# Performance work log

Measured on AMD Instinct MI355X. Metric: run time of the kernel, lower is better.

## Reference

```python
import jax, jax.numpy as jnp
import numpy as np

B, S, D = 2, 2048, 2048
H = 16
KV_RANK, Q_RANK = 512, 1536
NOPE, ROPE_D, VD = 128, 64, 128
QK_D = NOPE + ROPE_D  # 192


def _rope(t, positions):
    # t: (B, H, S, d) with d even; rotate-half RoPE, theta=10000
    d = t.shape[-1]
    inv_freq = 1.0 / (10000.0 ** (jnp.arange(0, d, 2, dtype=jnp.float32) / d))
    ang = positions.astype(jnp.float32)[:, None] * inv_freq  # (S, d//2)
    cos, sin = jnp.cos(ang), jnp.sin(ang)                    # (S, d//2)
    t1, t2 = t[..., : d // 2], t[..., d // 2 :]
    return jnp.concatenate([t1 * cos - t2 * sin, t2 * cos + t1 * sin], axis=-1)


def setup_inputs() -> dict:
    key = jax.random.key(0)
    ks = jax.random.split(key, 10)
    sc = 0.02
    return {
        "x": jax.random.normal(ks[0], (B, S, D), dtype=jnp.float32),
        "positions": jnp.arange(S, dtype=jnp.int32),
        # torch.nn.Linear weights are (out_features, in_features)
        "Wq_down": jax.random.normal(ks[1], (Q_RANK, D), dtype=jnp.float32) * sc,
        "Wq_up": jax.random.normal(ks[2], (H * NOPE, Q_RANK), dtype=jnp.float32) * sc,
        "Wq_rope": jax.random.normal(ks[3], (H * ROPE_D, Q_RANK), dtype=jnp.float32) * sc,
        "Wkv_down": jax.random.normal(ks[4], (KV_RANK, D), dtype=jnp.float32) * sc,
        "Wk_up": jax.random.normal(ks[5], (H * NOPE, KV_RANK), dtype=jnp.float32) * sc,
        "Wv_up": jax.random.normal(ks[6], (H * VD, KV_RANK), dtype=jnp.float32) * sc,
        "Wk_rope": jax.random.normal(ks[7], (ROPE_D, D), dtype=jnp.float32) * sc,
        "Wo": jax.random.normal(ks[8], (D, H * VD), dtype=jnp.float32) * sc,
    }


def reference(x, positions, Wq_down, Wq_up, Wq_rope, Wkv_down, Wk_up, Wv_up, Wk_rope, Wo):
    bsz, seq_len, _ = x.shape

    # Query path: low-rank down, then nope + rope up-projections
    c_q = x @ Wq_down.T                                             # (B, S, Q_RANK)
    q_c = (c_q @ Wq_up.T).reshape(bsz, seq_len, H, NOPE).transpose(0, 2, 1, 3)
    q_r = (c_q @ Wq_rope.T).reshape(bsz, seq_len, H, ROPE_D).transpose(0, 2, 1, 3)
    q_r = _rope(q_r, positions)
    q = jnp.concatenate([q_c, q_r], axis=-1)                        # (B, H, S, QK_D)

    # KV path: shared latent, single rope head broadcast to all heads
    c_kv = x @ Wkv_down.T                                           # (B, S, KV_RANK)
    k_c = (c_kv @ Wk_up.T).reshape(bsz, seq_len, H, NOPE).transpose(0, 2, 1, 3)
    v_c = (c_kv @ Wv_up.T).reshape(bsz, seq_len, H, VD).transpose(0, 2, 1, 3)
    k_r = (x @ Wk_rope.T).reshape(bsz, seq_len, 1, ROPE_D).transpose(0, 2, 1, 3)
    k_r = _rope(k_r, positions)
    k_r = jnp.broadcast_to(k_r, (bsz, H, seq_len, ROPE_D))
    k = jnp.concatenate([k_c, k_r], axis=-1)                        # (B, H, S, QK_D)

    # Causal SDPA, scale = 1/sqrt(total qk head dim)
    scale = 1.0 / math.sqrt(QK_D) if False else QK_D ** -0.5
    scores = jnp.einsum("bhqd,bhkd->bhqk", q, k) * scale
    causal = jnp.tril(jnp.ones((seq_len, seq_len), dtype=bool))
    scores = jnp.where(causal, scores, jnp.finfo(scores.dtype).min)
    attn = jax.nn.softmax(scores, axis=-1)
    out = jnp.einsum("bhqk,bhkd->bhqd", attn, v_c)                  # (B, H, S, VD)

    out = out.transpose(0, 2, 1, 3).reshape(bsz, seq_len, H * VD)
    return out @ Wo.T                                               # (B, S, D)
```

## Files before the change

kernel.cpp:

```cpp
#include <hip/hip_runtime.h>
#include <cmath>

#define SLEN 2048

typedef __bf16 bf16x8 __attribute__((ext_vector_type(8)));
typedef float  f32x4  __attribute__((ext_vector_type(4)));

__device__ inline void gld16(const void* g, void* l) {
    __builtin_amdgcn_global_load_lds(
        (const __attribute__((address_space(1))) void*)(uintptr_t)g,
        (__attribute__((address_space(3))) void*)(unsigned)(uintptr_t)l, 16, 0, 0);
}

struct CvArgs {
    const float* src[9];
    __bf16*      dst[9];
    long         cum[10];
};
__global__ __launch_bounds__(256)
void convert_all(CvArgs a) {
    long i8 = ((long)blockIdx.x * 256 + threadIdx.x) * 8;
    if (i8 >= a.cum[9]) return;
    int s = 0;
#pragma unroll
    for (int k = 1; k < 9; k++) if (i8 >= a.cum[k]) s = k;
    long loc = i8 - a.cum[s];
    const float* sp = a.src[s] + loc;
    float4 u0 = *(const float4*)(sp);
    float4 u1 = *(const float4*)(sp + 4);
    bf16x8 o;
    o[0] = (__bf16)u0.x; o[1] = (__bf16)u0.y; o[2] = (__bf16)u0.z; o[3] = (__bf16)u0.w;
    o[4] = (__bf16)u1.x; o[5] = (__bf16)u1.y; o[6] = (__bf16)u1.z; o[7] = (__bf16)u1.w;
    *(bf16x8*)(a.dst[s] + loc) = o;
}

struct Outs { __bf16* a; __bf16* b; __bf16* c; float* f; };

__global__ __launch_bounds__(256, 2)
void gemm_nt(const __bf16* __restrict__ A, const __bf16* __restrict__ B,
             Outs o, const int* __restrict__ positions,
             int M, int N, int K, int mode, float scale) {
    __shared__ __bf16 As[128 * 64];
    __shared__ __bf16 Bs[128 * 64];
    int tid = threadIdx.x;
    int wave = tid >> 6, lane = tid & 63;
    int lane15 = lane & 15, quad = lane >> 4;
    int ri = lane >> 3, ci = lane & 7;
    int cg = ci ^ ri;
    int m0 = blockIdx.x * 128, n0 = blockIdx.y * 128;
    int wm = (wave & 1) * 64, wn = (wave >> 1) * 64;
    f32x4 acc[4][4] = {};

    for (int k0 = 0; k0 < K; k0 += 64) {
#pragma unroll
        for (int t = 0; t < 4; t++) {
            int rr = wave * 32 + t * 8;
            int r = rr + ri;
            gld16(A + (size_t)(m0 + r) * K + k0 + cg * 8, As + rr * 64);
            int br = n0 + r; if (br > N - 1) br = N - 1;
            gld16(B + (size_t)br * K + k0 + cg * 8, Bs + rr * 64);
        }
        __syncthreads();
#pragma unroll
        for (int kk = 0; kk < 64; kk += 32) {
            int jb = kk >> 3;
            bf16x8 af[4], bfr[4];
#pragma unroll
            for (int mt = 0; mt < 4; mt++) {
                int rA = wm + mt * 16 + lane15;
                af[mt] = *(bf16x8*)(As + rA * 64 + (((jb + quad) ^ (rA & 7)) << 3));
            }
#pragma unroll
            for (int nt = 0; nt < 4; nt++) {
                int rB = wn + nt * 16 + lane15;
                bfr[nt] = *(bf16x8*)(Bs + rB * 64 + (((jb + quad) ^ (rB & 7)) << 3));
            }
#pragma unroll
            for (int mt = 0; mt < 4; mt++)
#pragma unroll
                for (int nt = 0; nt < 4; nt++)
                    acc[mt][nt] = __builtin_amdgcn_mfma_f32_16x16x32_bf16(
                        af[mt], bfr[nt], acc[mt][nt], 0, 0, 0);
        }
        __syncthreads();
    }

    const float KLOG = 13.287712379549449f / 32.0f;

    if (mode == 8 && n0 == 2048) {
        if (wn == 0) {
#pragma unroll
            for (int mt = 0; mt < 4; mt++) {
                int row = m0 + wm + mt * 16 + quad * 4;
#pragma unroll
                for (int nt = 0; nt < 2; nt++) {
                    int i = nt * 16 + lane15;
                    float inv = exp2f(-(float)i * KLOG);
#pragma unroll
                    for (int r = 0; r < 4; r++) {
                        int tok = row + r;
                        float p = (float)positions[tok & (SLEN - 1)];
                        float sn, cs; sincosf(p * inv, &sn, &cs);
                        float t1 = acc[mt][nt][r], t2 = acc[mt][nt + 2][r];
                        float rot1 = t1 * cs - t2 * sn;
                        float rot2 = t2 * cs + t1 * sn;
                        size_t ob = (size_t)tok * 3072 + 128;
#pragma unroll
                        for (int hh = 0; hh < 16; hh++) {
                            o.c[ob + hh * 192 + i]      = (__bf16)rot1;
                            o.c[ob + hh * 192 + 32 + i] = (__bf16)rot2;
                        }
                    }
                }
            }
        }
        return;
    }
    if (mode == 9 && n0 >= 2048) {
        int hh = (n0 + wn - 2048) >> 6;
#pragma unroll
        for (int mt = 0; mt < 4; mt++) {
            int row = m0 + wm + mt * 16 + quad * 4;
#pragma unroll
            for (int nt = 0; nt < 2; nt++) {
                int i = nt * 16 + lane15;
                float inv = exp2f(-(float)i * KLOG);
#pragma unroll
                for (int r = 0; r < 4; r++) {
                    int tok = row + r;
                    float p = (float)positions[tok & (SLEN - 1)];
                    float sn, cs; sincosf(p * inv, &sn, &cs);
                    float t1 = acc[mt][nt][r], t2 = acc[mt][nt + 2][r];
                    size_t ob = (size_t)tok * 3072 + hh * 192 + 128;
                    o.a[ob + i]      = (__bf16)((t1 * cs - t2 * sn) * scale);
                    o.a[ob + 32 + i] = (__bf16)((t2 * cs + t1 * sn) * scale);
                }
            }
        }
        return;
    }

#pragma unroll
    for (int mt = 0; mt < 4; mt++) {
        int row = m0 + wm + mt * 16 + quad * 4;
#pragma unroll
        for (int nt = 0; nt < 4; nt++) {
            int col = n0 + wn + nt * 16 + lane15;
            if (col < N) {
#pragma unroll
                for (int r = 0; r < 4; r++) {
                    float v = acc[mt][nt][r];
                    size_t rw = (size_t)(row + r);
                    if (mode == 2) {
                        o.f[rw * N + col] = v;
                    } else if (mode == 8) {
                        if (col < 1536) o.a[rw * 1536 + col] = (__bf16)v;
                        else            o.b[rw * 512 + col - 1536] = (__bf16)v;
                    } else if (mode == 9) {
                        o.a[rw * 3072 + (col >> 7) * 192 + (col & 127)] =
                            (__bf16)(v * scale);
                    } else {
                        if (col < 2048)
                            o.a[rw * 3072 + (col >> 7) * 192 + (col & 127)] = (__bf16)v;
                        else {
                            int d = col - 2048;
                            o.b[((size_t)d * 2 + (rw >> 11)) * 2048 + (rw & 2047)] = (__bf16)v;
                        }
                    }
                }
            }
        }
    }
}

__global__ __launch_bounds__(256, 2)
void mla_attn(const __bf16* __restrict__ Q, const __bf16* __restrict__ K,
              const __bf16* __restrict__ Vt, __bf16* __restrict__ O) {
    __shared__ __bf16 Ks[64 * 192];
    __shared__ __bf16 Vs[128 * 64];
    __shared__ __bf16 Ps[4][32][72];
    int tid = threadIdx.x, wave = tid >> 6, lane = tid & 63;
    int lane15 = lane & 15, quad = lane >> 4;
    int h = blockIdx.y, b = blockIdx.z;
    int x = blockIdx.x;
    int qt0 = (x & 1) ? (x >> 1) : (15 - (x >> 1));
    int qt = b ? (15 - qt0) : qt0;
    int q0 = qt * 128;
    const __bf16* Qb  = Q + (size_t)b * SLEN * 3072 + h * 192;
    const __bf16* Kb  = K + (size_t)b * SLEN * 3072 + h * 192;
    const __bf16* vtb = Vt + ((size_t)(h * 128) * 2 + b) * 2048;

    bf16x8 qf[2][6];
#pragma unroll
    for (int mt = 0; mt < 2; mt++) {
        int qrow = q0 + wave * 32 + mt * 16 + lane15;
#pragma unroll
        for (int kk = 0; kk < 6; kk++)
            qf[mt][kk] = *(const bf16x8*)(Qb + (size_t)qrow * 3072 + kk * 32 + quad * 8);
    }
    bf16x8 ones;
#pragma unroll
    for (int e = 0; e < 8; e++) ones[e] = (__bf16)1.0f;

    f32x4 o_acc[2][8] = {};
    float m_i[2][4], l_i[2][4];
#pragma unroll
    for (int mt = 0; mt < 2; mt++)
#pragma unroll
        for (int r = 0; r < 4; r++) { m_i[mt][r] = -3.0e38f; l_i[mt][r] = 0.0f; }

    for (int j0 = 0; j0 <= q0 + 64; j0 += 64) {
#pragma unroll
        for (int t = 0; t < 6; t++) {
            int sb = (wave * 6 + t) * 64;
            int slot = sb + lane;
            int r = slot / 24;
            int c = slot - r * 24;
            int cgk = (c & ~7) | ((c & 7) ^ (r & 7));
            gld16(Kb + (size_t)(j0 + r) * 3072 + cgk * 8, Ks + sb * 8);
        }
#pragma unroll
        for (int t = 0; t < 4; t++) {
            int sb = (wave * 4 + t) * 64;
            int slot = sb + lane;
            int r = slot >> 3, c = slot & 7;
            gld16(vtb + (size_t)r * 4096 + j0 + (c ^ (r & 7)) * 8, Vs + sb * 8);
        }
        __syncthreads();

        f32x4 acc[2][4] = {};
#pragma unroll
        for (int kk = 0; kk < 6; kk++) {
#pragma unroll
            for (int nt = 0; nt < 4; nt++) {
                int n = nt * 16 + lane15;
                int j = kk * 4 + quad;
                int cl = (j & ~7) | ((j & 7) ^ (n & 7));
                bf16x8 kf = *(bf16x8*)(Ks + n * 192 + cl * 8);
#pragma unroll
                for (int mt = 0; mt < 2; mt++)
                    acc[mt][nt] = __builtin_amdgcn_mfma_f32_16x16x32_bf16(
                        qf[mt][kk], kf, acc[mt][nt], 0, 0, 0);
            }
        }

        if (j0 >= q0) {
#pragma unroll
            for (int mt = 0; mt < 2; mt++) {
                int rowg = q0 + wave * 32 + mt * 16 + quad * 4;
#pragma unroll
                for (int nt = 0; nt < 4; nt++) {
                    int colg = j0 + nt * 16 + lane15;
#pragma unroll
                    for (int r = 0; r < 4; r++)
                        if (colg > rowg + r) acc[mt][nt][r] = -3.0e38f;
                }
            }
        }

        float mx[2][4];
        bool need = false;
#pragma unroll
        for (int mt = 0; mt < 2; mt++)
#pragma unroll
            for (int r = 0; r < 4; r++) {
                float v = fmaxf(fmaxf(acc[mt][0][r], acc[mt][1][r]),
                                fmaxf(acc[mt][2][r], acc[mt][3][r]));
                mx[mt][r] = v;
                need = need || (v > m_i[mt][r] + 24.0f);
            }
        if (__any(need)) {
#pragma unroll
            for (int mt = 0; mt < 2; mt++)
#pragma unroll
                for (int r = 0; r < 4; r++) {
                    float v = mx[mt][r];
#pragma unroll
                    for (int d = 8; d >= 1; d >>= 1) v = fmaxf(v, __shfl_xor(v, d));
                    float mn = fmaxf(m_i[mt][r], v);
                    float alpha = exp2f(m_i[mt][r] - mn);
                    m_i[mt][r] = mn;
                    l_i[mt][r] *= alpha;
#pragma unroll
                    for (int nt = 0; nt < 8; nt++) o_acc[mt][nt][r] *= alpha;
                }
        }

#pragma unroll
        for (int mt = 0; mt < 2; mt++)
#pragma unroll
            for (int r = 0; r < 4; r++)
#pragma unroll
                for (int nt = 0; nt < 4; nt++) {
                    float pp = exp2f(acc[mt][nt][r] - m_i[mt][r]);
                    Ps[wave][mt * 16 + quad * 4 + r][nt * 16 + lane15] = (__bf16)pp;
                }

        f32x4 rs[2] = {};
#pragma unroll
        for (int ks = 0; ks < 2; ks++) {
            bf16x8 pf[2];
#pragma unroll
            for (int mt = 0; mt < 2; mt++)
                pf[mt] = *(bf16x8*)(&Ps[wave][mt * 16 + lane15][ks * 32 + quad * 8]);
#pragma unroll
            for (int nt = 0; nt < 8; nt++) {
                int nn = nt * 16 + lane15;
                int j = ks * 4 + quad;
                bf16x8 vf = *(bf16x8*)(Vs + nn * 64 + (j ^ (nn & 7)) * 8);
#pragma unroll
                for (int mt = 0; mt < 2; mt++)
                    o_acc[mt][nt] = __builtin_amdgcn_mfma_f32_16x16x32_bf16(
                        pf[mt], vf, o_acc[mt][nt], 0, 0, 0);
            }
#pragma unroll
            for (int mt = 0; mt < 2; mt++)
                rs[mt] = __builtin_amdgcn_mfma_f32_16x16x32_bf16(
                    pf[mt], ones, rs[mt], 0, 0, 0);
        }
#pragma unroll
        for (int mt = 0; mt < 2; mt++)
#pragma unroll
            for (int r = 0; r < 4; r++) l_i[mt][r] += rs[mt][r];
        __syncthreads();
    }

    int tokb = b * SLEN + q0 + wave * 32 + quad * 4;
#pragma unroll
    for (int mt = 0; mt < 2; mt++) {
#pragma unroll
        for (int r = 0; r < 4; r++) {
            float inv_l = 1.0f / l_i[mt][r];
            int tok = tokb + mt * 16 + r;
#pragma unroll
            for (int nt = 0; nt < 8; nt++) {
                O[(size_t)tok * 2048 + h * 128 + nt * 16 + lane15] =
                    (__bf16)(o_acc[mt][nt][r] * inv_l);
            }
        }
    }
}

extern "C" void kernel_launch(void* const* d_in, const int* in_sizes, int n_in,
                              void* d_out, int out_size, void* d_ws, size_t ws_size,
                              hipStream_t stream) {
    (void)in_sizes; (void)n_in; (void)out_size; (void)ws_size;
    const int* pos = (const int*)d_in[1];
    float* out = (float*)d_out;

    char* ws = (char*)d_ws;
    size_t off = 0;
    auto alloc = [&](size_t bytes) {
        char* p = ws + off;
        off += (bytes + 255) & ~(size_t)255;
        return p;
    };
    __bf16* x_bf  = (__bf16*)alloc(8388608ull * 2);
    __bf16* Wcat1 = (__bf16*)alloc(4325376ull * 2);
    __bf16* Wcat2 = (__bf16*)alloc(4718592ull * 2);
    __bf16* Wcat3 = (__bf16*)alloc(4194304ull * 2);
    __bf16* Wob   = (__bf16*)alloc(4194304ull * 2);
    __bf16* c_q   = (__bf16*)alloc(4096ull * 1536 * 2);
    __bf16* c_kv  = (__bf16*)alloc(4096ull * 512 * 2);
    __bf16* v_t   = (__bf16*)alloc(4096ull * 2048 * 2);
    __bf16* q_all = (__bf16*)alloc(4096ull * 3072 * 2);
    __bf16* k_all = (__bf16*)alloc(4096ull * 3072 * 2);
    __bf16* attn_o = (__bf16*)c_q;

    const float scale_l2 = 1.4426950408889634f / sqrtf(192.0f);
    dim3 blk(256);

    CvArgs cv;
    cv.src[0] = (const float*)d_in[0]; cv.dst[0] = x_bf;
    cv.src[1] = (const float*)d_in[2]; cv.dst[1] = Wcat1;
    cv.src[2] = (const float*)d_in[5]; cv.dst[2] = Wcat1 + 3145728;
    cv.src[3] = (const float*)d_in[8]; cv.dst[3] = Wcat1 + 4194304;
    cv.src[4] = (const float*)d_in[3]; cv.dst[4] = Wcat2;
    cv.src[5] = (const float*)d_in[4]; cv.dst[5] = Wcat2 + 3145728;
    cv.src[6] = (const float*)d_in[6]; cv.dst[6] = Wcat3;
    cv.src[7] = (const float*)d_in[7]; cv.dst[7] = Wcat3 + 1048576;
    cv.src[8] = (const float*)d_in[9]; cv.dst[8] = Wob;
    long ns[9] = {8388608, 3145728, 1048576, 131072, 3145728, 1572864,
                  1048576, 1048576, 4194304};
    cv.cum[0] = 0;
    for (int i = 0; i < 9; i++) cv.cum[i + 1] = cv.cum[i] + ns[i];
    convert_all<<<dim3((unsigned)(cv.cum[9] / 2048)), blk, 0, stream>>>(cv);

    Outs o1 = { c_q, c_kv, k_all, nullptr };
    gemm_nt<<<dim3(32, 17), blk, 0, stream>>>(x_bf, Wcat1, o1, pos, 4096, 2112, 2048, 8, 1.0f);
    Outs o2 = { q_all, nullptr, nullptr, nullptr };
    gemm_nt<<<dim3(32, 24), blk, 0, stream>>>(c_q, Wcat2, o2, pos, 4096, 3072, 1536, 9, scale_l2);
    Outs o3 = { k_all, v_t, nullptr, nullptr };
    gemm_nt<<<dim3(32, 32), blk, 0, stream>>>(c_kv, Wcat3, o3, pos, 4096, 4096, 512, 10, 1.0f);
    mla_attn<<<dim3(16, 16, 2), blk, 0, stream>>>(q_all, k_all, v_t, attn_o);
    Outs o4 = { nullptr, nullptr, nullptr, out };
    gemm_nt<<<dim3(32, 16), blk, 0, stream>>>(attn_o, Wob, o4, pos, 4096, 2048, 2048, 2, 1.0f);
}
```

Before: 430.2 us.

## Split long causal query tiles across two blocks and merge partial softmax results

Query tiles 8-15 of the causal attention are split into two KV-range segments handled by separate blocks, giving 24 work items per head instead of 16. A table orders the items longest-first. Split segments write unnormalized bf16 partial outputs plus their running max and sum, and a new merge kernel combines them with log-sum-exp weights. This targets load imbalance and tail effects from uneven causal tile lengths, at the cost of an extra launch, extra global traffic for the partials, and bf16 rounding of the unnormalized partials.

```diff
diff --git a/kernel.cpp b/kernel.cpp
--- a/kernel.cpp
+++ b/kernel.cpp
@@ -173,19 +173,24 @@
     }
 }
 
+__constant__ int QT_TAB[24] = {15,15,7,14,14,6,13,13,12,12,5,11,11,10,10,4,9,9,8,8,3,2,1,0};
+__constant__ int SG_TAB[24] = {0,1,-1,0,1,-1,0,1,0,1,-1,0,1,0,1,-1,0,1,0,1,-1,-1,-1,-1};
+
 __global__ __launch_bounds__(256, 2)
 void mla_attn(const __bf16* __restrict__ Q, const __bf16* __restrict__ K,
-              const __bf16* __restrict__ Vt, __bf16* __restrict__ O) {
+              const __bf16* __restrict__ Vt, __bf16* __restrict__ O,
+              __bf16* __restrict__ po, float* __restrict__ ml) {
     __shared__ __bf16 Ks[64 * 192];
     __shared__ __bf16 Vs[128 * 64];
     __shared__ __bf16 Ps[4][32][72];
     int tid = threadIdx.x, wave = tid >> 6, lane = tid & 63;
     int lane15 = lane & 15, quad = lane >> 4;
     int h = blockIdx.y, b = blockIdx.z;
-    int x = blockIdx.x;
-    int qt0 = (x & 1) ? (x >> 1) : (15 - (x >> 1));
-    int qt = b ? (15 - qt0) : qt0;
+    int item = blockIdx.x;
+    int qt = QT_TAB[item], sg = SG_TAB[item];
     int q0 = qt * 128;
+    int ib = (sg == 1) ? qt + 1 : 0;
+    int ie = (sg == 0) ? qt + 1 : 2 * qt + 2;
     const __bf16* Qb  = Q + (size_t)b * SLEN * 3072 + h * 192;
     const __bf16* Kb  = K + (size_t)b * SLEN * 3072 + h * 192;
     const __bf16* vtb = Vt + ((size_t)(h * 128) * 2 + b) * 2048;
@@ -209,7 +214,8 @@
 #pragma unroll
         for (int r = 0; r < 4; r++) { m_i[mt][r] = -3.0e38f; l_i[mt][r] = 0.0f; }
 
-    for (int j0 = 0; j0 <= q0 + 64; j0 += 64) {
+    for (int ji = ib; ji < ie; ji++) {
+        int j0 = ji * 64;
 #pragma unroll
         for (int t = 0; t < 6; t++) {
             int sb = (wave * 6 + t) * 64;
@@ -325,19 +331,64 @@
         __syncthreads();
     }
 
-    int tokb = b * SLEN + q0 + wave * 32 + quad * 4;
-#pragma unroll
-    for (int mt = 0; mt < 2; mt++) {
-#pragma unroll
-        for (int r = 0; r < 4; r++) {
-            float inv_l = 1.0f / l_i[mt][r];
-            int tok = tokb + mt * 16 + r;
-#pragma unroll
-            for (int nt = 0; nt < 8; nt++) {
-                O[(size_t)tok * 2048 + h * 128 + nt * 16 + lane15] =
-                    (__bf16)(o_acc[mt][nt][r] * inv_l);
-            }
-        }
+    if (sg < 0) {
+        int tokb = b * SLEN + q0 + wave * 32 + quad * 4;
+#pragma unroll
+        for (int mt = 0; mt < 2; mt++)
+#pragma unroll
+            for (int r = 0; r < 4; r++) {
+                float inv_l = 1.0f / l_i[mt][r];
+                int tok = tokb + mt * 16 + r;
+#pragma unroll
+                for (int nt = 0; nt < 8; nt++)
+                    O[(size_t)tok * 2048 + h * 128 + nt * 16 + lane15] =
+                        (__bf16)(o_acc[mt][nt][r] * inv_l);
+            }
+    } else {
+        int tseg = (((b * 16 + h) * 8) + (qt - 8)) * 2 + sg;
+        __bf16* pb = po + (size_t)tseg * 16384;
+        float*  mb = ml + (size_t)tseg * 256;
+#pragma unroll
+        for (int mt = 0; mt < 2; mt++)
+#pragma unroll
+            for (int r = 0; r < 4; r++) {
+                int row = wave * 32 + mt * 16 + quad * 4 + r;
+#pragma unroll
+                for (int nt = 0; nt < 8; nt++)
+                    pb[(size_t)row * 128 + nt * 16 + lane15] = (__bf16)o_acc[mt][nt][r];
+                if (lane15 == 0) {
+                    mb[row * 2]     = m_i[mt][r];
+                    mb[row * 2 + 1] = l_i[mt][r];
+                }
+            }
+    }
+}
+
+__global__ __launch_bounds__(256)
+void attn_merge(const __bf16* __restrict__ po, const float* __restrict__ ml,
+                __bf16* __restrict__ O) {
+    int t = blockIdx.x;
+    int qti = t & 7, h = (t >> 3) & 15, b = t >> 7;
+    int row = threadIdx.x >> 1;
+    int cb = (threadIdx.x & 1) * 64;
+    int tok = b * SLEN + (8 + qti) * 128 + row;
+    size_t s0 = (size_t)(t * 2) * 16384 + (size_t)row * 128 + cb;
+    size_t s1 = s0 + 16384;
+    float2 a0 = *(const float2*)(ml + (size_t)(t * 2) * 256 + row * 2);
+    float2 a1 = *(const float2*)(ml + (size_t)(t * 2 + 1) * 256 + row * 2);
+    float mM = fmaxf(a0.x, a1.x);
+    float w0 = exp2f(a0.x - mM), w1 = exp2f(a1.x - mM);
+    float inv = 1.0f / (w0 * a0.y + w1 * a1.y);
+    w0 *= inv; w1 *= inv;
+#pragma unroll
+    for (int c = 0; c < 8; c++) {
+        bf16x8 v0 = *(const bf16x8*)(po + s0 + c * 8);
+        bf16x8 v1 = *(const bf16x8*)(po + s1 + c * 8);
+        bf16x8 o;
+#pragma unroll
+        for (int e = 0; e < 8; e++)
+            o[e] = (__bf16)(w0 * (float)v0[e] + w1 * (float)v1[e]);
+        *(bf16x8*)(O + (size_t)tok * 2048 + h * 128 + cb + c * 8) = o;
     }
 }
 
@@ -365,7 +416,9 @@
     __bf16* v_t   = (__bf16*)alloc(4096ull * 2048 * 2);
     __bf16* q_all = (__bf16*)alloc(4096ull * 3072 * 2);
     __bf16* k_all = (__bf16*)alloc(4096ull * 3072 * 2);
+    float*  ml    = (float*)alloc(512ull * 256 * 4);
     __bf16* attn_o = (__bf16*)c_q;
+    __bf16* po     = x_bf;
 
     const float scale_l2 = 1.4426950408889634f / sqrtf(192.0f);
     dim3 blk(256);
@@ -392,7 +445,8 @@
     gemm_nt<<<dim3(32, 24), blk, 0, stream>>>(c_q, Wcat2, o2, pos, 4096, 3072, 1536, 9, scale_l2);
     Outs o3 = { k_all, v_t, nullptr, nullptr };
     gemm_nt<<<dim3(32, 32), blk, 0, stream>>>(c_kv, Wcat3, o3, pos, 4096, 4096, 512, 10, 1.0f);
-    mla_attn<<<dim3(16, 16, 2), blk, 0, stream>>>(q_all, k_all, v_t, attn_o);
+    mla_attn<<<dim3(24, 16, 2), blk, 0, stream>>>(q_all, k_all, v_t, attn_o, po, ml);
+    attn_merge<<<dim3(256), blk, 0, stream>>>(po, ml, attn_o);
     Outs o4 = { nullptr, nullptr, nullptr, out };
     gemm_nt<<<dim3(32, 16), blk, 0, stream>>>(attn_o, Wob, o4, pos, 4096, 2048, 2048, 2, 1.0f);
 }
```

Measured after the change: 437.1 us. About the same (+1.6%).
